# Kernel optimization log

Hardware: AMD Instinct MI355X
Metric: run time of the kernel (lower is better)

Reference implementation:

```python
import jax, jax.numpy as jnp
import numpy as np

D_MODEL = 1024
HEADS = 16
D_K = D_MODEL // HEADS
D_FF = 4096
EPS = 1e-6


def setup_inputs() -> dict:
    key = jax.random.key(0)
    ks = jax.random.split(key, 20)
    B, S, D = 8, 1024, D_MODEL
    sc = 1.0 / np.sqrt(D)
    scf = 1.0 / np.sqrt(D_FF)
    inp = {
        "x": jax.random.normal(ks[0], (B, S, D), jnp.float32),
        "mask": jnp.ones((B, 1, 1, S), jnp.int32),
        "wq": jax.random.normal(ks[1], (D, D), jnp.float32) * sc,
        "bq": jnp.zeros((D,), jnp.float32),
        "wk": jax.random.normal(ks[2], (D, D), jnp.float32) * sc,
        "bk": jnp.zeros((D,), jnp.float32),
        "wv": jax.random.normal(ks[3], (D, D), jnp.float32) * sc,
        "bv": jnp.zeros((D,), jnp.float32),
        "wo": jax.random.normal(ks[4], (D, D), jnp.float32) * sc,
        "bo": jnp.zeros((D,), jnp.float32),
        "w1": jax.random.normal(ks[5], (D_FF, D), jnp.float32) * sc,
        "b1": jnp.zeros((D_FF,), jnp.float32),
        "w2": jax.random.normal(ks[6], (D, D_FF), jnp.float32) * scf,
        "b2": jnp.zeros((D,), jnp.float32),
        "g1": jnp.ones((D,), jnp.float32),
        "be1": jnp.zeros((D,), jnp.float32),
        "g2": jnp.ones((D,), jnp.float32),
        "be2": jnp.zeros((D,), jnp.float32),
    }
    return inp


def _layernorm(x, gamma, beta):
    # Faithful to custom LayerNorm: unbiased std (ddof=1), divide by (std+eps)
    mean = jnp.mean(x, axis=-1, keepdims=True)
    std = jnp.std(x, axis=-1, ddof=1, keepdims=True)
    return gamma * (x - mean) / (std + EPS) + beta


def _mha(x, mask, wq, bq, wk, bk, wv, bv, wo, bo):
    B, S, D = x.shape
    q = x @ wq.T + bq
    k = x @ wk.T + bk
    v = x @ wv.T + bv
    # [B,S,D] -> [B,H,S,dk]
    q = q.reshape(B, S, HEADS, D_K).transpose(0, 2, 1, 3)
    k = k.reshape(B, S, HEADS, D_K).transpose(0, 2, 1, 3)
    v = v.reshape(B, S, HEADS, D_K).transpose(0, 2, 1, 3)
    scores = jnp.einsum("bhqd,bhkd->bhqk", q, k) / np.sqrt(D_K).astype(np.float32)
    scores = jnp.where(mask == 0, jnp.float32(-1e9), scores)
    attn = jax.nn.softmax(scores, axis=-1)
    out = jnp.einsum("bhqk,bhkd->bhqd", attn, v)
    out = out.transpose(0, 2, 1, 3).reshape(B, S, D)
    return out @ wo.T + bo


def reference(x, mask, wq, bq, wk, bk, wv, bv, wo, bo, w1, b1, w2, b2, g1, be1, g2, be2):
    # residual 1: x + MHA(LN(x))
    h = _layernorm(x, g1, be1)
    x = x + _mha(h, mask, wq, bq, wk, bk, wv, bv, wo, bo)
    # residual 2: x + FFN(LN(x))
    h = _layernorm(x, g2, be2)
    ff = jax.nn.relu(h @ w1.T + b1) @ w2.T + b2
    return x + ff
```

## Files before the change

kernel.cpp:

```cpp
#include <hip/hip_runtime.h>

typedef __attribute__((ext_vector_type(8))) short short8;
typedef __attribute__((ext_vector_type(4))) short short4_t;
typedef __attribute__((ext_vector_type(4))) float floatx4;
typedef __attribute__((ext_vector_type(16))) float floatx16;

#define NTOK 8192
#define S_ 1024
#define DM 1024

__device__ __forceinline__ unsigned short f2b(float f) {
    union { float f; unsigned u; } v; v.f = f;
    unsigned r = v.u + 0x7FFF + ((v.u >> 16) & 1);
    return (unsigned short)(r >> 16);
}

__device__ __forceinline__ void gl_lds16(const void* g, void* l) {
    __builtin_amdgcn_global_load_lds((const __attribute__((address_space(1))) void*)g,
                                     (__attribute__((address_space(3))) void*)l, 16, 0, 0);
}

__global__ void cvt_f32_bf16(const float* __restrict__ src, unsigned short* __restrict__ dst, int n) {
    int i = (blockIdx.x * blockDim.x + threadIdx.x) * 4;
    if (i >= n) return;
    float4 v = *reinterpret_cast<const float4*>(src + i);
    short4_t o;
    o.x = (short)f2b(v.x); o.y = (short)f2b(v.y);
    o.z = (short)f2b(v.z); o.w = (short)f2b(v.w);
    *reinterpret_cast<short4_t*>(dst + i) = o;
}

__global__ void copy_f32(const float* __restrict__ src, float* __restrict__ dst, int n) {
    int i = (blockIdx.x * blockDim.x + threadIdx.x) * 4;
    if (i >= n) return;
    *reinterpret_cast<float4*>(dst + i) = *reinterpret_cast<const float4*>(src + i);
}

__global__ void mask_to_bias(const int* __restrict__ mask, float* __restrict__ mb,
                             int* __restrict__ flags, int n) {
    int i = blockIdx.x * blockDim.x + threadIdx.x;
    if (i < n) {
        const int m = mask[i];
        mb[i] = (m == 0) ? -1e9f : 0.f;
        if (m == 0) atomicOr(&flags[i >> 6], 1);
    }
}

__global__ __launch_bounds__(256) void ln_kernel(const float* __restrict__ x,
                                                 const float* __restrict__ g,
                                                 const float* __restrict__ be,
                                                 unsigned short* __restrict__ out) {
    const int row = blockIdx.x;
    const int t = threadIdx.x;
    const float4 xv = *reinterpret_cast<const float4*>(x + (size_t)row * DM + t * 4);
    float s = xv.x + xv.y + xv.z + xv.w;
#pragma unroll
    for (int off = 32; off > 0; off >>= 1) s += __shfl_down(s, off);
    __shared__ float red[8];
    const int wid = t >> 6, lane = t & 63;
    if (lane == 0) red[wid] = s;
    __syncthreads();
    const float mean = (red[0] + red[1] + red[2] + red[3]) * (1.f / 1024.f);
    const float dx = xv.x - mean, dy = xv.y - mean, dz = xv.z - mean, dw = xv.w - mean;
    float ss = dx * dx + dy * dy + dz * dz + dw * dw;
#pragma unroll
    for (int off = 32; off > 0; off >>= 1) ss += __shfl_down(ss, off);
    if (lane == 0) red[4 + wid] = ss;
    __syncthreads();
    const float var = (red[4] + red[5] + red[6] + red[7]) * (1.f / 1023.f);
    const float inv = 1.f / (sqrtf(var) + 1e-6f);
    const float4 gv = *reinterpret_cast<const float4*>(g + t * 4);
    const float4 bv = *reinterpret_cast<const float4*>(be + t * 4);
    short4_t o;
    o.x = (short)f2b(gv.x * dx * inv + bv.x);
    o.y = (short)f2b(gv.y * dy * inv + bv.y);
    o.z = (short)f2b(gv.z * dz * inv + bv.z);
    o.w = (short)f2b(gv.w * dw * inv + bv.w);
    *reinterpret_cast<short4_t*>(out + (size_t)row * DM + t * 4) = o;
}

template <int EPI>
__global__ __launch_bounds__(256, 2) void gemm_bt(const unsigned short* __restrict__ A,
                                                  const unsigned short* __restrict__ Bm,
                                                  const float* __restrict__ bias,
                                                  const float* __restrict__ res,
                                                  void* __restrict__ outp,
                                                  int M, int N, int K, int tilesX) {
    __shared__ __align__(16) unsigned short lds[2][2][8192];
    const int t = threadIdx.x;
    const int lane = t & 63, wid = t >> 6;
    const int wr = wid >> 1, wc = wid & 1;

    const int bid = blockIdx.x;
    const int xcd = bid & 7;
    const int lid = bid >> 3;
    const int sid = lid >> 5;
    const int off = lid & 31;
    const int gsid = sid * 8 + xcd;
    const int supercols = tilesX >> 2;
    const int srow = gsid / supercols;
    const int scol = gsid - srow * supercols;
    const int rowBase = (srow * 8 + (off >> 2)) * 128;
    const int colBase = (scol * 4 + (off & 3)) * 128;

    const int NT = K >> 6;
    const int lr31 = lane & 31;
    const int kh = lane >> 5;

    const unsigned short* Ag[4];
    const unsigned short* Bg[4];
#pragma unroll
    for (int j = 0; j < 4; ++j) {
        const int L = j * 256 + t;
        const int r = L >> 3;
        const int c = ((L & 7) ^ (r & 7)) * 8;
        Ag[j] = A + (size_t)(rowBase + r) * K + c;
        Bg[j] = Bm + (size_t)(colBase + r) * K + c;
    }

    floatx16 acc[2][2] = {};

#pragma unroll
    for (int j = 0; j < 4; ++j) gl_lds16(Ag[j], &lds[0][0][j * 2048 + wid * 512]);
#pragma unroll
    for (int j = 0; j < 4; ++j) gl_lds16(Bg[j], &lds[0][1][j * 2048 + wid * 512]);
#pragma unroll
    for (int j = 0; j < 4; ++j) { Ag[j] += 64; Bg[j] += 64; }

    int cur = 0;
    for (int tt = 0; tt < NT; ++tt) {
        if (tt + 1 < NT) {
#pragma unroll
            for (int j = 0; j < 4; ++j)
                gl_lds16(Ag[j], &lds[cur ^ 1][0][j * 2048 + wid * 512]);
#pragma unroll
            for (int j = 0; j < 4; ++j)
                gl_lds16(Bg[j], &lds[cur ^ 1][1][j * 2048 + wid * 512]);
#pragma unroll
            for (int j = 0; j < 4; ++j) { Ag[j] += 64; Bg[j] += 64; }
            asm volatile("s_waitcnt vmcnt(8)" ::: "memory");
        } else {
            asm volatile("s_waitcnt vmcnt(0)" ::: "memory");
        }
        __builtin_amdgcn_s_barrier();
        __builtin_amdgcn_sched_barrier(0);
        const unsigned short* Ab = &lds[cur][0][0];
        const unsigned short* Bb = &lds[cur][1][0];
#pragma unroll
        for (int ks = 0; ks < 4; ++ks) {
            short8 af[2], bfr[2];
#pragma unroll
            for (int mf = 0; mf < 2; ++mf) {
                const int r = wr * 64 + mf * 32 + lr31;
                const int cp = (ks * 2 + kh) ^ (r & 7);
                af[mf] = *reinterpret_cast<const short8*>(&Ab[r * 64 + cp * 8]);
            }
#pragma unroll
            for (int nf = 0; nf < 2; ++nf) {
                const int r = wc * 64 + nf * 32 + lr31;
                const int cp = (ks * 2 + kh) ^ (r & 7);
                bfr[nf] = *reinterpret_cast<const short8*>(&Bb[r * 64 + cp * 8]);
            }
            __builtin_amdgcn_s_setprio(1);
#pragma unroll
            for (int mf = 0; mf < 2; ++mf)
#pragma unroll
                for (int nf = 0; nf < 2; ++nf)
                    acc[mf][nf] = __builtin_amdgcn_mfma_f32_32x32x16_bf16(af[mf], bfr[nf], acc[mf][nf], 0, 0, 0);
            __builtin_amdgcn_s_setprio(0);
        }
        __builtin_amdgcn_sched_barrier(0);
        __builtin_amdgcn_s_barrier();
        cur ^= 1;
    }

    const int rbw = rowBase + wr * 64;
    const int cbw = colBase + wc * 64;
    const int lc31 = lane & 31;
    if (EPI == 4) {
        unsigned short* qh = (unsigned short*)outp;
        const float SC2 = 0.18033688f;
#pragma unroll
        for (int nf = 0; nf < 2; ++nf) {
            const int c = cbw + nf * 32 + lc31;
            const float bn = bias[c];
            const int sect = c >> 10;
            const int hh = (c >> 6) & 15;
            const int dd = c & 63;
            const float scl = (sect == 0) ? SC2 : 1.f;
#pragma unroll
            for (int mf = 0; mf < 2; ++mf) {
#pragma unroll
                for (int rg = 0; rg < 4; ++rg) {
                    const int r0 = rbw + mf * 32 + rg * 8 + 4 * kh;
                    const int bb = r0 >> 10, ss = r0 & 1023;
                    if (sect == 2) {
                        short4_t pk;
#pragma unroll
                        for (int j = 0; j < 4; ++j) pk[j] = (short)f2b(acc[mf][nf][rg * 4 + j] + bn);
                        *reinterpret_cast<short4_t*>(
                            &qh[16777216 + ((size_t)((bb * 16 + hh) * 64 + dd)) * 1024 + ss]) = pk;
                    } else {
                        unsigned short* base = qh + sect * 8388608;
#pragma unroll
                        for (int j = 0; j < 4; ++j)
                            base[((size_t)((bb * 16 + hh) * 1024 + ss + j)) * 64 + dd] =
                                f2b((acc[mf][nf][rg * 4 + j] + bn) * scl);
                    }
                }
            }
        }
        return;
    }
#pragma unroll
    for (int nf = 0; nf < 2; ++nf) {
        const int c = cbw + nf * 32 + lc31;
        const float bn = bias[c];
#pragma unroll
        for (int mf = 0; mf < 2; ++mf) {
#pragma unroll
            for (int rg = 0; rg < 4; ++rg) {
#pragma unroll
                for (int j = 0; j < 4; ++j) {
                    const int r = rbw + mf * 32 + rg * 8 + 4 * kh + j;
                    ((float*)outp)[(size_t)r * N + c] =
                        acc[mf][nf][rg * 4 + j] + bn + res[(size_t)r * N + c];
                }
            }
        }
    }
}

__global__ __launch_bounds__(512, 2) void gemm256p(const unsigned short* __restrict__ A,
                                                   const unsigned short* __restrict__ Bm,
                                                   const float* __restrict__ bias,
                                                   unsigned short* __restrict__ outp,
                                                   int M, int N, int K, int tilesX) {
    __shared__ __align__(16) unsigned short Abuf[2][16384];
    __shared__ __align__(16) unsigned short Bbuf[2][16384];
    const int t = threadIdx.x;
    const int lane = t & 63, wid = t >> 6;
    const int wr = wid >> 2, wc = wid & 3;

    const int bid = blockIdx.x;
    const int xcd = bid & 7;
    const int lid = bid >> 3;
    const int sid = lid >> 5;
    const int off = lid & 31;
    const int gsid = sid * 8 + xcd;
    const int supercols = tilesX >> 2;
    const int srow = gsid / supercols;
    const int scol = gsid - srow * supercols;
    const int rowBase = (srow * 8 + (off >> 2)) * 256;
    const int colBase = (scol * 4 + (off & 3)) * 256;

    const int NT = K >> 6;
    const int lr31 = lane & 31;
    const int kh = lane >> 5;
    const int x7 = lane & 7;

    const int tr = t >> 3;
    const int c0 = ((t & 7) ^ (tr & 7)) * 8;
    const int ldst = t * 8;
    const unsigned short* Asrc[4];
    const unsigned short* Bsrc[4];
#pragma unroll
    for (int u = 0; u < 4; ++u) {
        Asrc[u] = A + (size_t)(rowBase + u * 64 + tr) * K + c0;
        Bsrc[u] = Bm + (size_t)(colBase + u * 64 + tr) * K + c0;
    }

#define STG_A(b_, kk_)                                                      \
    do {                                                                    \
        _Pragma("unroll") for (int u = 0; u < 4; ++u)                       \
            gl_lds16(Asrc[u] + (kk_), &Abuf[b_][u * 4096 + ldst]);          \
    } while (0)
#define STG_B(b_, kk_)                                                      \
    do {                                                                    \
        _Pragma("unroll") for (int u = 0; u < 4; ++u)                       \
            gl_lds16(Bsrc[u] + (kk_), &Bbuf[b_][u * 4096 + ldst]);          \
    } while (0)
#define READQ(q_, af_, bf_)                                                             \
    do {                                                                                \
        _Pragma("unroll") for (int mf = 0; mf < 4; ++mf) {                              \
            const int rho = wr * 128 + mf * 32 + lr31;                                  \
            (af_)[mf] = *reinterpret_cast<const short8*>(                               \
                &Abuf[cur][rho * 64 + ((2 * (q_) + kh) ^ x7) * 8]);                     \
        }                                                                               \
        _Pragma("unroll") for (int nf = 0; nf < 2; ++nf) {                              \
            const int rho = wc * 64 + nf * 32 + lr31;                                   \
            (bf_)[nf] = *reinterpret_cast<const short8*>(                               \
                &Bbuf[cur][rho * 64 + ((2 * (q_) + kh) ^ x7) * 8]);                     \
        }                                                                               \
    } while (0)
#define MFMAQ(af_, bf_)                                                                 \
    do {                                                                                \
        __builtin_amdgcn_s_setprio(1);                                                  \
        _Pragma("unroll") for (int mf = 0; mf < 4; ++mf)                                \
            _Pragma("unroll") for (int nf = 0; nf < 2; ++nf)                            \
                acc[mf][nf] = __builtin_amdgcn_mfma_f32_32x32x16_bf16((af_)[mf],        \
                                  (bf_)[nf], acc[mf][nf], 0, 0, 0);                     \
        __builtin_amdgcn_s_setprio(0);                                                  \
    } while (0)

    floatx16 acc[4][2] = {};

    STG_A(0, 0);
    STG_B(0, 0);

    short8 afA[4], bfA[2], afB[4], bfB[2];
    for (int kt = 0; kt < NT; ++kt) {
        const int cur = kt & 1, nxt = cur ^ 1;
        const bool pf = (kt + 1 < NT);
        const int kkn = (pf ? kt + 1 : kt) << 6;
        __builtin_amdgcn_s_barrier();
        if (pf) STG_A(nxt, kkn);
        if (pf) asm volatile("s_waitcnt vmcnt(4)" ::: "memory");
        else    asm volatile("s_waitcnt vmcnt(0)" ::: "memory");
        __builtin_amdgcn_sched_barrier(0);
        READQ(0, afA, bfA);
        if (pf) STG_B(nxt, kkn);
        READQ(1, afB, bfB);
        MFMAQ(afA, bfA);
        READQ(2, afA, bfA);
        MFMAQ(afB, bfB);
        READQ(3, afB, bfB);
        MFMAQ(afA, bfA);
        MFMAQ(afB, bfB);
    }
#undef STG_A
#undef STG_B
#undef READQ
#undef MFMAQ

    const int rbw = rowBase + wr * 128;
    const int cbw = colBase + wc * 64;
    const int lc31 = lane & 31;
#pragma unroll
    for (int nf = 0; nf < 2; ++nf) {
        const int c = cbw + nf * 32 + lc31;
        const float bn = bias[c];
#pragma unroll
        for (int mf = 0; mf < 4; ++mf) {
#pragma unroll
            for (int rg = 0; rg < 4; ++rg) {
                const int r0 = rbw + mf * 32 + rg * 8 + 4 * kh;
#pragma unroll
                for (int j = 0; j < 4; ++j) {
                    const float v = fmaxf(acc[mf][nf][rg * 4 + j] + bn, 0.f);
                    outp[(size_t)(r0 + j) * N + c] = f2b(v);
                }
            }
        }
    }
}

__global__ __launch_bounds__(256) void attn_mfma(const unsigned short* __restrict__ Qh,
                                                 const unsigned short* __restrict__ Kh,
                                                 const unsigned short* __restrict__ Vt,
                                                 const float* __restrict__ mbias,
                                                 const int* __restrict__ mflags,
                                                 unsigned short* __restrict__ out) {
    __shared__ __align__(16) unsigned short Kbuf[2][4096];
    __shared__ __align__(16) unsigned short Vbuf[2][4096];
    __shared__ __align__(16) unsigned short Pbuf[4][16][72];
    __shared__ __align__(16) float mk[1024];
    const int t = threadIdx.x;
    const int w = t >> 6, l = t & 63;
    const int g = l >> 4, q16 = l & 15;
    const int x7 = q16 & 7;
    const int bid = blockIdx.x;
    const int swz = (bid & 7) * 256 + (bid >> 3);
    const int bh = swz >> 4, qb = swz & 15;
    const int b = bh >> 4, h = bh & 15;

    const size_t qbase = ((size_t)bh * 1024 + qb * 64 + w * 16 + q16) * 64;
    const short8 qf0 = *reinterpret_cast<const short8*>(Qh + qbase + g * 8);
    const short8 qf1 = *reinterpret_cast<const short8*>(Qh + qbase + 32 + g * 8);

    const int r0 = t >> 3;
    const int c0 = ((t & 7) ^ (r0 & 7)) * 8;
    const unsigned short* Kg = Kh + (size_t)bh * 65536 + r0 * 64 + c0;
    const unsigned short* Vg = Vt + (size_t)bh * 65536 + r0 * 1024 + c0;

#define ATTN_STAGE(bi, kc_)                                                        \
    do {                                                                           \
        gl_lds16(Kg + (kc_) * 4096, &Kbuf[bi][w * 512]);                           \
        gl_lds16(Kg + (kc_) * 4096 + 2048, &Kbuf[bi][2048 + w * 512]);             \
        gl_lds16(Vg + (kc_) * 64, &Vbuf[bi][w * 512]);                             \
        gl_lds16(Vg + (kc_) * 64 + 32768, &Vbuf[bi][2048 + w * 512]);              \
    } while (0)

    gl_lds16(mbias + b * 1024 + t * 4, &mk[w * 256]);
    ATTN_STAGE(0, 0);

    floatx4 oacc[4] = {};
    floatx4 loacc = {};
    short8 ones;
#pragma unroll
    for (int j = 0; j < 8; ++j) ones[j] = (short)0x3F80;

    int cur = 0;
    for (int kc = 0; kc < 16; ++kc) {
        if (kc < 15) {
            ATTN_STAGE(cur ^ 1, kc + 1);
            asm volatile("s_waitcnt vmcnt(4)" ::: "memory");
        } else {
            asm volatile("s_waitcnt vmcnt(0)" ::: "memory");
        }
        __builtin_amdgcn_s_barrier();
        __builtin_amdgcn_sched_barrier(0);
        const unsigned short* Kb = Kbuf[cur];
        const unsigned short* Vb = Vbuf[cur];

        floatx4 st[4] = {};
        __builtin_amdgcn_s_setprio(1);
#pragma unroll
        for (int t4 = 0; t4 < 4; ++t4) {
            const int row = t4 * 16 + q16;
            const short8 kf0 = *reinterpret_cast<const short8*>(&Kb[row * 64 + (g ^ x7) * 8]);
            const short8 kf1 = *reinterpret_cast<const short8*>(&Kb[row * 64 + ((4 + g) ^ x7) * 8]);
            st[t4] = __builtin_amdgcn_mfma_f32_16x16x32_bf16(kf0, qf0, st[t4], 0, 0, 0);
            st[t4] = __builtin_amdgcn_mfma_f32_16x16x32_bf16(kf1, qf1, st[t4], 0, 0, 0);
        }
        __builtin_amdgcn_s_setprio(0);

        if (mflags[b * 16 + kc]) {
#pragma unroll
            for (int t4 = 0; t4 < 4; ++t4) {
                const float4 mbv = *reinterpret_cast<const float4*>(&mk[kc * 64 + t4 * 16 + g * 4]);
#pragma unroll
                for (int r = 0; r < 4; ++r) st[t4][r] += ((const float*)&mbv)[r];
            }
        }
#pragma unroll
        for (int t4 = 0; t4 < 4; ++t4) {
            const float p0 = __builtin_exp2f(st[t4][0]);
            const float p1 = __builtin_exp2f(st[t4][1]);
            const float p2 = __builtin_exp2f(st[t4][2]);
            const float p3 = __builtin_exp2f(st[t4][3]);
            unsigned u0, u1;
            asm("v_cvt_pk_bf16_f32 %0, %1, %2" : "=v"(u0) : "v"(p0), "v"(p1));
            asm("v_cvt_pk_bf16_f32 %0, %1, %2" : "=v"(u1) : "v"(p2), "v"(p3));
            uint2 pr; pr.x = u0; pr.y = u1;
            *reinterpret_cast<uint2*>(&Pbuf[w][q16][t4 * 16 + g * 4]) = pr;
        }

        const short8 pf0 = *reinterpret_cast<const short8*>(&Pbuf[w][q16][g * 8]);
        const short8 pf1 = *reinterpret_cast<const short8*>(&Pbuf[w][q16][32 + g * 8]);
        __builtin_amdgcn_s_setprio(1);
        loacc = __builtin_amdgcn_mfma_f32_16x16x32_bf16(pf0, ones, loacc, 0, 0, 0);
        loacc = __builtin_amdgcn_mfma_f32_16x16x32_bf16(pf1, ones, loacc, 0, 0, 0);
#pragma unroll
        for (int n = 0; n < 4; ++n) {
            const int row = n * 16 + q16;
            const short8 vf0 = *reinterpret_cast<const short8*>(&Vb[row * 64 + (g ^ x7) * 8]);
            const short8 vf1 = *reinterpret_cast<const short8*>(&Vb[row * 64 + ((4 + g) ^ x7) * 8]);
            oacc[n] = __builtin_amdgcn_mfma_f32_16x16x32_bf16(pf0, vf0, oacc[n], 0, 0, 0);
            oacc[n] = __builtin_amdgcn_mfma_f32_16x16x32_bf16(pf1, vf1, oacc[n], 0, 0, 0);
        }
        __builtin_amdgcn_s_setprio(0);
        __builtin_amdgcn_sched_barrier(0);
        __builtin_amdgcn_s_barrier();
        cur ^= 1;
    }
#undef ATTN_STAGE

    const size_t obase = ((size_t)b * S_ + qb * 64 + w * 16) * 1024 + h * 64;
#pragma unroll
    for (int r = 0; r < 4; ++r) {
        const float invr = 1.f / loacc[r];
        const size_t orow = obase + (size_t)(g * 4 + r) * 1024;
#pragma unroll
        for (int n = 0; n < 4; ++n)
            out[orow + n * 16 + q16] = f2b(oacc[n][r] * invr);
    }
}

extern "C" void kernel_launch(void* const* d_in, const int* in_sizes, int n_in,
                              void* d_out, int out_size, void* d_ws, size_t ws_size,
                              hipStream_t stream) {
    const float* x   = (const float*)d_in[0];
    const int*  mask = (const int*)d_in[1];
    const float* wq  = (const float*)d_in[2];
    const float* bq  = (const float*)d_in[3];
    const float* wk  = (const float*)d_in[4];
    const float* bk  = (const float*)d_in[5];
    const float* wv  = (const float*)d_in[6];
    const float* bv  = (const float*)d_in[7];
    const float* wo  = (const float*)d_in[8];
    const float* bo  = (const float*)d_in[9];
    const float* w1  = (const float*)d_in[10];
    const float* b1  = (const float*)d_in[11];
    const float* w2  = (const float*)d_in[12];
    const float* b2  = (const float*)d_in[13];
    const float* g1  = (const float*)d_in[14];
    const float* be1 = (const float*)d_in[15];
    const float* g2  = (const float*)d_in[16];
    const float* be2 = (const float*)d_in[17];

    char* ws = (char*)d_ws;
    unsigned short* wqkv_bf = (unsigned short*)(ws);
    unsigned short* wo_bf   = (unsigned short*)(ws + 6291456);
    unsigned short* w1_bf   = (unsigned short*)(ws + 8388608);
    unsigned short* w2_bf   = (unsigned short*)(ws + 16777216);
    float*          bqkv    = (float*)(ws + 25165824);
    float*          mbias   = (float*)(ws + 25178112);
    int*            mflags  = (int*)(ws + 25210880);
    unsigned short* h_bf    = (unsigned short*)(ws + 25214976);
    float*          x1      = (float*)(ws + 41992192);
    unsigned short* attn_bf = (unsigned short*)(ws + 75546624);
    unsigned short* qkvh    = (unsigned short*)(ws + 92323840);
    unsigned short* ff1_bf  = (unsigned short*)(ws + 92323840);

    cvt_f32_bf16<<<1024, 256, 0, stream>>>(wq, wqkv_bf, 1048576);
    cvt_f32_bf16<<<1024, 256, 0, stream>>>(wk, wqkv_bf + 1048576, 1048576);
    cvt_f32_bf16<<<1024, 256, 0, stream>>>(wv, wqkv_bf + 2097152, 1048576);
    cvt_f32_bf16<<<1024, 256, 0, stream>>>(wo, wo_bf, 1048576);
    cvt_f32_bf16<<<4096, 256, 0, stream>>>(w1, w1_bf, 4194304);
    cvt_f32_bf16<<<4096, 256, 0, stream>>>(w2, w2_bf, 4194304);
    copy_f32<<<1, 256, 0, stream>>>(bq, bqkv, 1024);
    copy_f32<<<1, 256, 0, stream>>>(bk, bqkv + 1024, 1024);
    copy_f32<<<1, 256, 0, stream>>>(bv, bqkv + 2048, 1024);
    hipMemsetAsync(mflags, 0, 128 * sizeof(int), stream);
    mask_to_bias<<<32, 256, 0, stream>>>(mask, mbias, mflags, 8192);

    ln_kernel<<<NTOK, 256, 0, stream>>>(x, g1, be1, h_bf);
    gemm_bt<4><<<24 * 64, 256, 0, stream>>>(h_bf, wqkv_bf, bqkv, nullptr, qkvh, NTOK, 3072, 1024, 24);
    attn_mfma<<<2048, 256, 0, stream>>>(qkvh, qkvh + 8388608, qkvh + 16777216, mbias, mflags, attn_bf);
    gemm_bt<1><<<8 * 64, 256, 0, stream>>>(attn_bf, wo_bf, bo, x, x1, NTOK, 1024, 1024, 8);
    ln_kernel<<<NTOK, 256, 0, stream>>>(x1, g2, be2, h_bf);
    gemm256p<<<512, 512, 0, stream>>>(h_bf, w1_bf, b1, ff1_bf, NTOK, 4096, 1024, 16);
    gemm_bt<1><<<8 * 64, 256, 0, stream>>>(ff1_bf, w2_bf, b2, x1, (float*)d_out, NTOK, 1024, 4096, 8);
}
```

Before: 380.2 us.

## Restructure GEMM main loop into quarter-phased load/compute schedule with split staging

```diff
diff --git a/kernel.cpp b/kernel.cpp
--- a/kernel.cpp
+++ b/kernel.cpp
@@ -259,79 +259,92 @@
     const int kh = lane >> 5;
     const int x7 = lane & 7;
 
-    const int tr = t >> 3;
-    const int c0 = ((t & 7) ^ (tr & 7)) * 8;
+    const int rho_s = t >> 3;
+    const int csrc = ((t & 7) ^ (rho_s & 7)) * 8;
     const int ldst = t * 8;
-    const unsigned short* Asrc[4];
-    const unsigned short* Bsrc[4];
-#pragma unroll
-    for (int u = 0; u < 4; ++u) {
-        Asrc[u] = A + (size_t)(rowBase + u * 64 + tr) * K + c0;
-        Bsrc[u] = Bm + (size_t)(colBase + u * 64 + tr) * K + c0;
-    }
-
-#define STG_A(b_, kk_)                                                      \
-    do {                                                                    \
-        _Pragma("unroll") for (int u = 0; u < 4; ++u)                       \
-            gl_lds16(Asrc[u] + (kk_), &Abuf[b_][u * 4096 + ldst]);          \
+    const unsigned short* Bs_[2][2];
+    const unsigned short* As_[2][2];
+#pragma unroll
+    for (int h = 0; h < 2; ++h)
+#pragma unroll
+        for (int j = 0; j < 2; ++j) {
+            const int rr = rho_s + j * 64;
+            Bs_[h][j] = Bm + (size_t)(colBase + h * 128 + rr) * K + csrc;
+            As_[h][j] = A + (size_t)(rowBase + ((rr >> 6) * 128 + h * 64 + (rr & 63))) * K + csrc;
+        }
+
+#define STG_BH(h_, b_, kk_)                                                   \
+    do {                                                                      \
+        gl_lds16(Bs_[h_][0] + (kk_), &Bbuf[b_][(h_)*8192 + ldst]);            \
+        gl_lds16(Bs_[h_][1] + (kk_), &Bbuf[b_][(h_)*8192 + 4096 + ldst]);     \
     } while (0)
-#define STG_B(b_, kk_)                                                      \
-    do {                                                                    \
-        _Pragma("unroll") for (int u = 0; u < 4; ++u)                       \
-            gl_lds16(Bsrc[u] + (kk_), &Bbuf[b_][u * 4096 + ldst]);          \
+#define STG_AH(h_, b_, kk_)                                                   \
+    do {                                                                      \
+        gl_lds16(As_[h_][0] + (kk_), &Abuf[b_][(h_)*8192 + ldst]);            \
+        gl_lds16(As_[h_][1] + (kk_), &Abuf[b_][(h_)*8192 + 4096 + ldst]);     \
     } while (0)
-#define READQ(q_, af_, bf_)                                                             \
-    do {                                                                                \
-        _Pragma("unroll") for (int mf = 0; mf < 4; ++mf) {                              \
-            const int rho = wr * 128 + mf * 32 + lr31;                                  \
-            (af_)[mf] = *reinterpret_cast<const short8*>(                               \
-                &Abuf[cur][rho * 64 + ((2 * (q_) + kh) ^ x7) * 8]);                     \
-        }                                                                               \
-        _Pragma("unroll") for (int nf = 0; nf < 2; ++nf) {                              \
-            const int rho = wc * 64 + nf * 32 + lr31;                                   \
-            (bf_)[nf] = *reinterpret_cast<const short8*>(                               \
-                &Bbuf[cur][rho * 64 + ((2 * (q_) + kh) ^ x7) * 8]);                     \
-        }                                                                               \
-    } while (0)
-#define MFMAQ(af_, bf_)                                                                 \
-    do {                                                                                \
-        __builtin_amdgcn_s_setprio(1);                                                  \
-        _Pragma("unroll") for (int mf = 0; mf < 4; ++mf)                                \
-            _Pragma("unroll") for (int nf = 0; nf < 2; ++nf)                            \
-                acc[mf][nf] = __builtin_amdgcn_mfma_f32_32x32x16_bf16((af_)[mf],        \
-                                  (bf_)[nf], acc[mf][nf], 0, 0, 0);                     \
-        __builtin_amdgcn_s_setprio(0);                                                  \
-    } while (0)
 
     floatx16 acc[4][2] = {};
 
-    STG_A(0, 0);
-    STG_B(0, 0);
-
-    short8 afA[4], bfA[2], afB[4], bfB[2];
+    STG_BH(0, 0, 0); STG_BH(1, 0, 0); STG_AH(0, 0, 0); STG_AH(1, 0, 0);
+    asm volatile("s_waitcnt vmcnt(0)" ::: "memory");
+    __builtin_amdgcn_s_barrier();
+
     for (int kt = 0; kt < NT; ++kt) {
         const int cur = kt & 1, nxt = cur ^ 1;
         const bool pf = (kt + 1 < NT);
         const int kkn = (pf ? kt + 1 : kt) << 6;
-        __builtin_amdgcn_s_barrier();
-        if (pf) STG_A(nxt, kkn);
-        if (pf) asm volatile("s_waitcnt vmcnt(4)" ::: "memory");
-        else    asm volatile("s_waitcnt vmcnt(0)" ::: "memory");
-        __builtin_amdgcn_sched_barrier(0);
-        READQ(0, afA, bfA);
-        if (pf) STG_B(nxt, kkn);
-        READQ(1, afB, bfB);
-        MFMAQ(afA, bfA);
-        READQ(2, afA, bfA);
-        MFMAQ(afB, bfB);
-        READQ(3, afB, bfB);
-        MFMAQ(afA, bfA);
-        MFMAQ(afB, bfB);
-    }
-#undef STG_A
-#undef STG_B
-#undef READQ
-#undef MFMAQ
+        short8 bfr[2][4];
+#pragma unroll
+        for (int q = 0; q < 4; ++q) {
+            short8 af[4];
+            {
+                const int rho = wr * 64 + (q & 1) * 32 + lr31;
+                const unsigned short* Ab = &Abuf[cur][(q >> 1) * 8192];
+#pragma unroll
+                for (int s = 0; s < 4; ++s)
+                    af[s] = *reinterpret_cast<const short8*>(
+                        &Ab[rho * 64 + ((2 * s + kh) ^ x7) * 8]);
+            }
+            if (q == 0) {
+#pragma unroll
+                for (int nf = 0; nf < 2; ++nf) {
+                    const int gcol = wc * 64 + nf * 32 + lr31;
+                    const unsigned short* Bb = &Bbuf[cur][(gcol >> 7) * 8192];
+                    const int rho = gcol & 127;
+#pragma unroll
+                    for (int s = 0; s < 4; ++s)
+                        bfr[nf][s] = *reinterpret_cast<const short8*>(
+                            &Bb[rho * 64 + ((2 * s + kh) ^ x7) * 8]);
+                }
+            }
+            if (pf) {
+                if (q == 0) STG_BH(0, nxt, kkn);
+                if (q == 1) STG_BH(1, nxt, kkn);
+                if (q == 2) STG_AH(0, nxt, kkn);
+                if (q == 3) STG_AH(1, nxt, kkn);
+            }
+            __builtin_amdgcn_s_barrier();
+            asm volatile("s_waitcnt lgkmcnt(0)" ::: "memory");
+            __builtin_amdgcn_sched_barrier(0);
+            __builtin_amdgcn_s_setprio(1);
+#pragma unroll
+            for (int s = 0; s < 4; ++s)
+#pragma unroll
+                for (int nf = 0; nf < 2; ++nf)
+                    acc[q][nf] = __builtin_amdgcn_mfma_f32_32x32x16_bf16(af[s], bfr[nf][s], acc[q][nf], 0, 0, 0);
+            __builtin_amdgcn_s_setprio(0);
+            __builtin_amdgcn_sched_barrier(0);
+            if (q == 1) {
+                if (pf) asm volatile("s_waitcnt vmcnt(4)" ::: "memory");
+                else    asm volatile("s_waitcnt vmcnt(0)" ::: "memory");
+            }
+            if (q == 3 && pf) asm volatile("s_waitcnt vmcnt(2)" ::: "memory");
+            __builtin_amdgcn_s_barrier();
+        }
+    }
+#undef STG_AH
+#undef STG_BH
 
     const int rbw = rowBase + wr * 128;
     const int cbw = colBase + wc * 64;
@@ -341,13 +354,13 @@
         const int c = cbw + nf * 32 + lc31;
         const float bn = bias[c];
 #pragma unroll
-        for (int mf = 0; mf < 4; ++mf) {
+        for (int q = 0; q < 4; ++q) {
 #pragma unroll
             for (int rg = 0; rg < 4; ++rg) {
-                const int r0 = rbw + mf * 32 + rg * 8 + 4 * kh;
+                const int r0 = rbw + q * 32 + rg * 8 + 4 * kh;
 #pragma unroll
                 for (int j = 0; j < 4; ++j) {
-                    const float v = fmaxf(acc[mf][nf][rg * 4 + j] + bn, 0.f);
+                    const float v = fmaxf(acc[q][nf][rg * 4 + j] + bn, 0.f);
                     outp[(size_t)(r0 + j) * N + c] = f2b(v);
                 }
             }
```

Measured after the change: 380.5 us. No clear change (+0.1%).
